# Kernel tuning notes

Hardware: AMD Instinct MI355X
Metric: run time of the kernel (lower is better)

The kernel has to match this reference:

```python
import jax, jax.numpy as jnp
import numpy as np

N = 1024      # num_nodes
D = 64        # input/hidden/output feature dim
IDX = 64      # idx_dim
H = 8         # msg MLP width
L = 3         # num_layers


def setup_inputs() -> dict:
    key = jax.random.key(0)
    ks = jax.random.split(key, 10)
    return {
        "y": jax.random.normal(ks[0], (N, D), jnp.float32),
        "adj": jax.random.uniform(ks[1], (N, N), jnp.float32),
        "adj_deriv": jax.random.normal(ks[2], (N, N), jnp.float32),
        "t_grad": jax.random.normal(ks[3], (N, N), jnp.float32),
        "idx_emb": jax.random.normal(ks[4], (N, IDX), jnp.float32),
        # stacked params for the two msg MLPs (index 0 = adj, 1 = adj_derivative)
        "msg_W1": jax.random.normal(ks[5], (2, H, 2 * IDX + 1), jnp.float32) / np.float32(np.sqrt(2 * IDX + 1)),
        "msg_b1": jnp.zeros((2, H), jnp.float32),
        "msg_W2": jax.random.normal(ks[6], (2, H, H), jnp.float32) / np.float32(np.sqrt(H)),
        "msg_b2": jnp.zeros((2, H), jnp.float32),
        "msg_W3": jax.random.normal(ks[7], (2, 1, H), jnp.float32) / np.float32(np.sqrt(H)),
        "msg_b3": jnp.zeros((2, 1), jnp.float32),
        # per-layer fusion weights: [A@x, A.T@x, dA@x, dA.T@x, x] -> 5 matrices
        "gnn_W": jax.random.normal(ks[8], (L, 5, D, D), jnp.float32) / np.float32(np.sqrt(D)),
        "gnn_b": jnp.zeros((L, D), jnp.float32),
    }


def _msg_mlp(a, idx_emb, W1, b1, W2, b2, W3, b3):
    # Edge-wise 2-hidden-layer relu MLP over concat([a_ij, emb_i, emb_j]).
    # Split W1 so the [N,N,2*IDX+1] concat is never materialized.
    w_a = W1[:, 0]                 # [H]
    w_i = W1[:, 1:1 + IDX]         # [H, IDX]
    w_j = W1[:, 1 + IDX:]          # [H, IDX]
    row = idx_emb @ w_i.T          # [N, H]
    col = idx_emb @ w_j.T          # [N, H]
    h = jax.nn.relu(a[:, :, None] * w_a + row[:, None, :] + col[None, :, :] + b1)  # [N,N,H]
    h = jax.nn.relu(jnp.einsum('nmh,kh->nmk', h, W2) + b2)                          # [N,N,H]
    out = jnp.einsum('nmh,oh->nmo', h, W3) + b3                                     # [N,N,1]
    return out[..., 0]


def reference(y, adj, adj_deriv, t_grad, idx_emb, msg_W1, msg_b1, msg_W2, msg_b2,
              msg_W3, msg_b3, gnn_W, gnn_b):
    # enc_idx=True: reweight adjacency and its derivative with the edge-wise MLPs
    a = _msg_mlp(adj, idx_emb, msg_W1[0], msg_b1[0], msg_W2[0], msg_b2[0], msg_W3[0], msg_b3[0])
    ad = _msg_mlp(adj_deriv, idx_emb, msg_W1[1], msg_b1[1], msg_W2[1], msg_b2[1], msg_W3[1], msg_b3[1])

    x = y
    for l in range(L):
        W, b = gnn_W[l], gnn_b[l]
        x = ((a @ x) @ W[0] + (a.T @ x) @ W[1]
             + (ad @ x) @ W[2] + (ad.T @ x) @ W[3]
             + x @ W[4] + b)
        if l < L - 1:
            x = jax.nn.relu(x)

    tg = jnp.mean(t_grad, axis=0)          # [N]
    return tg[:, None] * x                 # einsum('i,ij->ij')
```

## Files before the change

kernel.cpp:

```cpp
#include <hip/hip_runtime.h>

typedef __attribute__((ext_vector_type(8))) short bf16x8;
typedef __attribute__((ext_vector_type(4))) float f32x4;
typedef __attribute__((ext_vector_type(4))) unsigned short us4;

__device__ __forceinline__ unsigned short f2bf(float f) {
    unsigned int u = __builtin_bit_cast(unsigned int, f);
    unsigned int r = (u + 0x7fffu + ((u >> 16) & 1u)) >> 16;
    return (unsigned short)r;
}

__global__ __launch_bounds__(256) void k_aux(
    const float* __restrict__ idx_emb, const float* __restrict__ msg_W1,
    float* __restrict__ rc,
    const float* __restrict__ t_grad, float* __restrict__ tg,
    const float* __restrict__ y, unsigned short* __restrict__ xbf,
    const float* __restrict__ gnn_W, unsigned short* __restrict__ WbfT) {
    __shared__ float red[4][64];
    int bx = blockIdx.x, t = threadIdx.x;
    if (bx < 128) {
        int tid = bx * 256 + t;
        int h = tid & 7, n = (tid >> 3) & 1023, t_ = (tid >> 13) & 1, k = tid >> 14;
        const float* wv = msg_W1 + k * 1032 + h * 129 + 1 + t_ * 64;
        const float* e = idx_emb + n * 64;
        float s = 0.f;
#pragma unroll
        for (int d = 0; d < 64; ++d) s += e[d] * wv[d];
        rc[(k * 2 + t_) * 8192 + n * 8 + h] = s;
    } else if (bx < 144) {
        int jl = t & 63, sg = t >> 6;
        int j = (bx - 128) * 64 + jl;
        float acc = 0.f;
        for (int i = 0; i < 256; ++i) acc += t_grad[(sg * 256 + i) * 1024 + j];
        red[sg][jl] = acc;
        __syncthreads();
        if (sg == 0)
            tg[j] = (red[0][jl] + red[1][jl] + red[2][jl] + red[3][jl]) * (1.f / 1024.f);
    } else if (bx < 160) {
        int base = (bx - 144) * 4096 + t;
#pragma unroll
        for (int p = 0; p < 16; ++p) xbf[base + p * 256] = f2bf(y[base + p * 256]);
    } else if (bx < 175) {
        int wi = bx - 160;
        const float* src = gnn_W + wi * 4096;
        unsigned short* dst = WbfT + wi * 4096;
        int c = t & 63, dg = t >> 6;
#pragma unroll
        for (int p = 0; p < 16; ++p) {
            int d = dg + p * 4;
            dst[c * 64 + d] = f2bf(src[d * 64 + c]);
        }
    }
}

__global__ __launch_bounds__(256) void k_msgcvt(
    const float* __restrict__ adj, const float* __restrict__ adj_deriv,
    const float* __restrict__ W1, const float* __restrict__ b1,
    const float* __restrict__ W2, const float* __restrict__ b2,
    const float* __restrict__ W3, const float* __restrict__ b3,
    const float* __restrict__ rc, unsigned short* __restrict__ Abf) {
    int mt = blockIdx.x, nt = blockIdx.y, z = blockIdx.z;
    const float* A = z ? adj_deriv : adj;
    unsigned short* D0 = Abf + z * 2097152;
    unsigned short* D1 = D0 + 1048576;
    int k = z;

    float wa[8], b1v[8], w2[64], b2v[8], w3v[8];
#pragma unroll
    for (int h = 0; h < 8; ++h) {
        wa[h]  = W1[k * 1032 + h * 129];
        b1v[h] = b1[k * 8 + h];
        b2v[h] = b2[k * 8 + h];
        w3v[h] = W3[k * 8 + h];
    }
#pragma unroll
    for (int i = 0; i < 64; ++i) w2[i] = W2[k * 64 + i];
    float b3v = b3[k];

    int t = threadIdx.x;
    int c = t & 63, rg = t >> 6;
    const float* colp = rc + (k * 2 + 1) * 8192 + (mt * 64 + c) * 8;
    float cm[8];
    *(float4*)&cm[0] = *(const float4*)colp;
    *(float4*)&cm[4] = *(const float4*)(colp + 4);
    const float* rowp = rc + (k * 2) * 8192 + (nt * 64) * 8;

    __shared__ unsigned short tile[64][65];
#pragma unroll
    for (int p = 0; p < 16; ++p) {
        int r = rg + 4 * p;
        float av = A[(nt * 64 + r) * 1024 + mt * 64 + c];
        float rn[8];
        *(float4*)&rn[0] = *(const float4*)(rowp + r * 8);
        *(float4*)&rn[4] = *(const float4*)(rowp + r * 8 + 4);
        float h1[8];
#pragma unroll
        for (int h = 0; h < 8; ++h) {
            float v = av * wa[h] + rn[h] + cm[h] + b1v[h];
            h1[h] = v > 0.f ? v : 0.f;
        }
        float o = b3v;
#pragma unroll
        for (int kk = 0; kk < 8; ++kk) {
            float s = b2v[kk];
#pragma unroll
            for (int h = 0; h < 8; ++h) s += h1[h] * w2[kk * 8 + h];
            s = s > 0.f ? s : 0.f;
            o += s * w3v[kk];
        }
        unsigned short us = f2bf(o);
        D0[(nt * 64 + r) * 1024 + mt * 64 + c] = us;
        tile[r][c] = us;
    }
    __syncthreads();
#pragma unroll
    for (int p = 0; p < 16; ++p) {
        int r = rg + 4 * p;
        D1[(mt * 64 + r) * 1024 + nt * 64 + c] = tile[c][r];
    }
}

template<int L>
__global__ __launch_bounds__(256) void k_layer(
    const unsigned short* __restrict__ Abf,
    const unsigned short* __restrict__ xbf,
    const float* __restrict__ Pin, const float* __restrict__ u4in,
    const float* __restrict__ bprev,
    const unsigned short* __restrict__ WT,
    float* __restrict__ u4out, float* __restrict__ Pout) {
    int nt = blockIdx.x, ms = blockIdx.y;
    int t = threadIdx.x, w = t >> 6, l64 = t & 63;
    int lr = l64 & 15, lk = l64 >> 4, klo = 8 * lk;
    int m0 = ms * 64;
    __shared__ unsigned short uTs[16384];
    __shared__ unsigned short xs[4096];

    if constexpr (L == 0) {
#pragma unroll
        for (int p = 0; p < 2; ++p) {
            int e = (t + p * 256) * 8;
            *(bf16x8*)&xs[e] = *(const bf16x8*)&xbf[m0 * 64 + e];
        }
    } else {
#pragma unroll
        for (int p = 0; p < 4; ++p) {
            int q = t + p * 256;
            int row = q >> 4, c4 = (q & 15) * 4;
            int gi = (m0 + row) * 64 + c4;
            float4 acc4 = *(const float4*)&u4in[gi];
            float4 b4 = *(const float4*)&bprev[c4];
            acc4.x += b4.x; acc4.y += b4.y; acc4.z += b4.z; acc4.w += b4.w;
#pragma unroll
            for (int s = 0; s < 16; ++s) {
                float4 pv = *(const float4*)&Pin[s * 65536 + gi];
                acc4.x += pv.x; acc4.y += pv.y; acc4.z += pv.z; acc4.w += pv.w;
            }
            us4 pk;
            pk[0] = f2bf(fmaxf(acc4.x, 0.f));
            pk[1] = f2bf(fmaxf(acc4.y, 0.f));
            pk[2] = f2bf(fmaxf(acc4.z, 0.f));
            pk[3] = f2bf(fmaxf(acc4.w, 0.f));
            *(us4*)&xs[row * 64 + c4] = pk;
        }
    }
    __syncthreads();

    int mloc = w * 16 + lr;
    bf16x8 xa0 = *(const bf16x8*)&xs[mloc * 64 + klo];
    bf16x8 xa1 = *(const bf16x8*)&xs[mloc * 64 + 32 + klo];
    int njmax = (nt == 0) ? 5 : 4;
    for (int j = 0; j < njmax; ++j) {
        f32x4 au[4];
#pragma unroll
        for (int cf = 0; cf < 4; ++cf) au[cf] = (f32x4){0.f, 0.f, 0.f, 0.f};
#pragma unroll
        for (int cf = 0; cf < 4; ++cf) {
            bf16x8 wf0 = *(const bf16x8*)&WT[(j * 64 + cf * 16 + lr) * 64 + klo];
            bf16x8 wf1 = *(const bf16x8*)&WT[(j * 64 + cf * 16 + lr) * 64 + 32 + klo];
            au[cf] = __builtin_amdgcn_mfma_f32_16x16x32_bf16(xa0, wf0, au[cf], 0, 0, 0);
            au[cf] = __builtin_amdgcn_mfma_f32_16x16x32_bf16(xa1, wf1, au[cf], 0, 0, 0);
        }
        if (j < 4) {
#pragma unroll
            for (int cf = 0; cf < 4; ++cf) {
                int cc = cf * 16 + lr;
                us4 pk;
                pk[0] = f2bf(au[cf][0]); pk[1] = f2bf(au[cf][1]);
                pk[2] = f2bf(au[cf][2]); pk[3] = f2bf(au[cf][3]);
                int off = ((j * 64 + cc) * 64 + w * 16 + lk * 4) * 2;
                *(us4*)((char*)uTs + (off ^ ((cc & 7) << 4))) = pk;
            }
        } else {
#pragma unroll
            for (int cf = 0; cf < 4; ++cf)
#pragma unroll
                for (int r = 0; r < 4; ++r)
                    u4out[(m0 + w * 16 + lk * 4 + r) * 64 + cf * 16 + lr] = au[cf][r];
        }
    }
    __syncthreads();

    f32x4 acc[4];
#pragma unroll
    for (int cf = 0; cf < 4; ++cf) acc[cf] = (f32x4){0.f, 0.f, 0.f, 0.f};
    int arow = nt * 64 + w * 16 + lr;
#pragma unroll
    for (int j = 0; j < 4; ++j) {
#pragma unroll
        for (int kk = 0; kk < 2; ++kk) {
            bf16x8 af = *(const bf16x8*)&Abf[j * 1048576 + arow * 1024 + m0 + kk * 32 + klo];
#pragma unroll
            for (int cf = 0; cf < 4; ++cf) {
                int cc = cf * 16 + lr;
                int off = ((j * 64 + cc) * 64 + kk * 32 + klo) * 2;
                bf16x8 bfr = *(const bf16x8*)((char*)uTs + (off ^ ((cc & 7) << 4)));
                acc[cf] = __builtin_amdgcn_mfma_f32_16x16x32_bf16(af, bfr, acc[cf], 0, 0, 0);
            }
        }
    }
    float* Pp = Pout + ms * 65536;
    int nbase = nt * 64 + w * 16 + lk * 4;
#pragma unroll
    for (int cf = 0; cf < 4; ++cf)
#pragma unroll
        for (int r = 0; r < 4; ++r)
            Pp[(nbase + r) * 64 + cf * 16 + lr] = acc[cf][r];
}

__global__ void k_final(const float* __restrict__ P, const float* __restrict__ u4,
                        const float* __restrict__ b, const float* __restrict__ tg,
                        float* __restrict__ out) {
    int idx = blockIdx.x * 256 + threadIdx.x;
    int n = idx >> 6, c = idx & 63;
    float s = u4[idx] + b[c];
#pragma unroll
    for (int k = 0; k < 16; ++k) s += P[k * 65536 + idx];
    out[idx] = tg[n] * s;
}

extern "C" void kernel_launch(void* const* d_in, const int* in_sizes, int n_in,
                              void* d_out, int out_size, void* d_ws, size_t ws_size,
                              hipStream_t stream) {
    const float* y         = (const float*)d_in[0];
    const float* adj       = (const float*)d_in[1];
    const float* adj_deriv = (const float*)d_in[2];
    const float* t_grad    = (const float*)d_in[3];
    const float* idx_emb   = (const float*)d_in[4];
    const float* msg_W1    = (const float*)d_in[5];
    const float* msg_b1    = (const float*)d_in[6];
    const float* msg_W2    = (const float*)d_in[7];
    const float* msg_b2    = (const float*)d_in[8];
    const float* msg_W3    = (const float*)d_in[9];
    const float* msg_b3    = (const float*)d_in[10];
    const float* gnn_W     = (const float*)d_in[11];
    const float* gnn_b     = (const float*)d_in[12];
    float* outp = (float*)d_out;

    float* ws = (float*)d_ws;
    float* rc   = ws;
    float* tg   = ws + 32768;
    float* u4A  = ws + 33792;
    float* u4B  = ws + 99328;
    float* PA   = ws + 164864;
    float* PB   = ws + 1213440;
    unsigned short* xbf  = (unsigned short*)(ws + 2262016);
    unsigned short* WbfT = (unsigned short*)(ws + 2294784);
    unsigned short* Abf  = (unsigned short*)(ws + 2325504);

    k_aux<<<175, 256, 0, stream>>>(idx_emb, msg_W1, rc, t_grad, tg,
                                   y, xbf, gnn_W, WbfT);
    k_msgcvt<<<dim3(16, 16, 2), 256, 0, stream>>>(adj, adj_deriv,
                                                  msg_W1, msg_b1, msg_W2, msg_b2,
                                                  msg_W3, msg_b3, rc, Abf);
    k_layer<0><<<dim3(16, 16), 256, 0, stream>>>(Abf, xbf, PA, u4A, gnn_b,
                                                 WbfT, u4A, PA);
    k_layer<1><<<dim3(16, 16), 256, 0, stream>>>(Abf, xbf, PA, u4A, gnn_b,
                                                 WbfT + 20480, u4B, PB);
    k_layer<2><<<dim3(16, 16), 256, 0, stream>>>(Abf, xbf, PB, u4B, gnn_b + 64,
                                                 WbfT + 40960, u4A, PA);
    k_final<<<256, 256, 0, stream>>>(PA, u4A, gnn_b + 128, tg, outp);
}
```

Baseline: 73.10 us.

## Widen layer K-split to 256 columns per block, fold self term into partials

Each layer block now covers 256 source nodes in four chunks instead of 64, so the grid shrinks from 16x16 to 16x4 and the partial-sum buffers shrink from 16 slices to 4. The separate u4 (x@W4) output is gone. The diagonal block computes the self term straight into its accumulator, which reduces reduction traffic in the next layer and in the final kernel. In exchange there are only 64 blocks on a GPU with many CUs, so occupancy and parallelism drop, and each block does more serial work with extra barriers.

```diff
diff --git a/kernel.cpp b/kernel.cpp
--- a/kernel.cpp
+++ b/kernel.cpp
@@ -121,37 +121,35 @@
 }
 
 template<int L>
-__global__ __launch_bounds__(256) void k_layer(
+__global__ __launch_bounds__(256) void k_g(
     const unsigned short* __restrict__ Abf,
     const unsigned short* __restrict__ xbf,
-    const float* __restrict__ Pin, const float* __restrict__ u4in,
+    const unsigned short* __restrict__ WT,
     const float* __restrict__ bprev,
-    const unsigned short* __restrict__ WT,
-    float* __restrict__ u4out, float* __restrict__ Pout) {
+    const float* __restrict__ Pin,
+    float* __restrict__ Pout) {
     int nt = blockIdx.x, ms = blockIdx.y;
     int t = threadIdx.x, w = t >> 6, l64 = t & 63;
     int lr = l64 & 15, lk = l64 >> 4, klo = 8 * lk;
-    int m0 = ms * 64;
+    __shared__ unsigned short xs[16384];
     __shared__ unsigned short uTs[16384];
-    __shared__ unsigned short xs[4096];
 
     if constexpr (L == 0) {
 #pragma unroll
-        for (int p = 0; p < 2; ++p) {
-            int e = (t + p * 256) * 8;
-            *(bf16x8*)&xs[e] = *(const bf16x8*)&xbf[m0 * 64 + e];
+        for (int p = 0; p < 8; ++p) {
+            int q = t + p * 256;
+            int e = q * 8;
+            *(bf16x8*)&xs[e] = *(const bf16x8*)&xbf[ms * 16384 + e];
         }
     } else {
 #pragma unroll
-        for (int p = 0; p < 4; ++p) {
+        for (int p = 0; p < 16; ++p) {
             int q = t + p * 256;
             int row = q >> 4, c4 = (q & 15) * 4;
-            int gi = (m0 + row) * 64 + c4;
-            float4 acc4 = *(const float4*)&u4in[gi];
-            float4 b4 = *(const float4*)&bprev[c4];
-            acc4.x += b4.x; acc4.y += b4.y; acc4.z += b4.z; acc4.w += b4.w;
-#pragma unroll
-            for (int s = 0; s < 16; ++s) {
+            int gi = (ms * 256 + row) * 64 + c4;
+            float4 acc4 = *(const float4*)&bprev[c4];
+#pragma unroll
+            for (int s = 0; s < 4; ++s) {
                 float4 pv = *(const float4*)&Pin[s * 65536 + gi];
                 acc4.x += pv.x; acc4.y += pv.y; acc4.z += pv.z; acc4.w += pv.w;
             }
@@ -165,22 +163,42 @@
     }
     __syncthreads();
 
-    int mloc = w * 16 + lr;
-    bf16x8 xa0 = *(const bf16x8*)&xs[mloc * 64 + klo];
-    bf16x8 xa1 = *(const bf16x8*)&xs[mloc * 64 + 32 + klo];
-    int njmax = (nt == 0) ? 5 : 4;
-    for (int j = 0; j < njmax; ++j) {
-        f32x4 au[4];
-#pragma unroll
-        for (int cf = 0; cf < 4; ++cf) au[cf] = (f32x4){0.f, 0.f, 0.f, 0.f};
-#pragma unroll
-        for (int cf = 0; cf < 4; ++cf) {
-            bf16x8 wf0 = *(const bf16x8*)&WT[(j * 64 + cf * 16 + lr) * 64 + klo];
-            bf16x8 wf1 = *(const bf16x8*)&WT[(j * 64 + cf * 16 + lr) * 64 + 32 + klo];
-            au[cf] = __builtin_amdgcn_mfma_f32_16x16x32_bf16(xa0, wf0, au[cf], 0, 0, 0);
-            au[cf] = __builtin_amdgcn_mfma_f32_16x16x32_bf16(xa1, wf1, au[cf], 0, 0, 0);
-        }
-        if (j < 4) {
+    f32x4 acc[4];
+#pragma unroll
+    for (int cf = 0; cf < 4; ++cf) acc[cf] = (f32x4){0.f, 0.f, 0.f, 0.f};
+
+    if (ms == (nt >> 2)) {
+        const unsigned short* W4 = WT + 16384;
+        int xrow = (nt & 3) * 64 + w * 16 + lr;
+#pragma unroll
+        for (int kk = 0; kk < 2; ++kk) {
+            bf16x8 af = *(const bf16x8*)&xs[xrow * 64 + kk * 32 + klo];
+#pragma unroll
+            for (int cf = 0; cf < 4; ++cf) {
+                bf16x8 bfr = *(const bf16x8*)&W4[(cf * 16 + lr) * 64 + kk * 32 + klo];
+                acc[cf] = __builtin_amdgcn_mfma_f32_16x16x32_bf16(af, bfr, acc[cf], 0, 0, 0);
+            }
+        }
+    }
+
+    int arow = nt * 64 + w * 16 + lr;
+    for (int ch = 0; ch < 4; ++ch) {
+        if (ch > 0) __syncthreads();
+        int mloc = ch * 64 + w * 16 + lr;
+        bf16x8 xa0 = *(const bf16x8*)&xs[mloc * 64 + klo];
+        bf16x8 xa1 = *(const bf16x8*)&xs[mloc * 64 + 32 + klo];
+#pragma unroll
+        for (int j = 0; j < 4; ++j) {
+            f32x4 au[4];
+#pragma unroll
+            for (int cf = 0; cf < 4; ++cf) au[cf] = (f32x4){0.f, 0.f, 0.f, 0.f};
+#pragma unroll
+            for (int cf = 0; cf < 4; ++cf) {
+                bf16x8 wf0 = *(const bf16x8*)&WT[(j * 64 + cf * 16 + lr) * 64 + klo];
+                bf16x8 wf1 = *(const bf16x8*)&WT[(j * 64 + cf * 16 + lr) * 64 + 32 + klo];
+                au[cf] = __builtin_amdgcn_mfma_f32_16x16x32_bf16(xa0, wf0, au[cf], 0, 0, 0);
+                au[cf] = __builtin_amdgcn_mfma_f32_16x16x32_bf16(xa1, wf1, au[cf], 0, 0, 0);
+            }
 #pragma unroll
             for (int cf = 0; cf < 4; ++cf) {
                 int cc = cf * 16 + lr;
@@ -190,34 +208,26 @@
                 int off = ((j * 64 + cc) * 64 + w * 16 + lk * 4) * 2;
                 *(us4*)((char*)uTs + (off ^ ((cc & 7) << 4))) = pk;
             }
-        } else {
-#pragma unroll
-            for (int cf = 0; cf < 4; ++cf)
-#pragma unroll
-                for (int r = 0; r < 4; ++r)
-                    u4out[(m0 + w * 16 + lk * 4 + r) * 64 + cf * 16 + lr] = au[cf][r];
-        }
-    }
-    __syncthreads();
-
-    f32x4 acc[4];
-#pragma unroll
-    for (int cf = 0; cf < 4; ++cf) acc[cf] = (f32x4){0.f, 0.f, 0.f, 0.f};
-    int arow = nt * 64 + w * 16 + lr;
-#pragma unroll
-    for (int j = 0; j < 4; ++j) {
-#pragma unroll
-        for (int kk = 0; kk < 2; ++kk) {
-            bf16x8 af = *(const bf16x8*)&Abf[j * 1048576 + arow * 1024 + m0 + kk * 32 + klo];
-#pragma unroll
-            for (int cf = 0; cf < 4; ++cf) {
-                int cc = cf * 16 + lr;
-                int off = ((j * 64 + cc) * 64 + kk * 32 + klo) * 2;
-                bf16x8 bfr = *(const bf16x8*)((char*)uTs + (off ^ ((cc & 7) << 4)));
-                acc[cf] = __builtin_amdgcn_mfma_f32_16x16x32_bf16(af, bfr, acc[cf], 0, 0, 0);
-            }
-        }
-    }
+        }
+        __syncthreads();
+
+        int m0 = ms * 256 + ch * 64;
+#pragma unroll
+        for (int j = 0; j < 4; ++j) {
+#pragma unroll
+            for (int kk = 0; kk < 2; ++kk) {
+                bf16x8 af = *(const bf16x8*)&Abf[j * 1048576 + arow * 1024 + m0 + kk * 32 + klo];
+#pragma unroll
+                for (int cf = 0; cf < 4; ++cf) {
+                    int cc = cf * 16 + lr;
+                    int off = ((j * 64 + cc) * 64 + kk * 32 + klo) * 2;
+                    bf16x8 bfr = *(const bf16x8*)((char*)uTs + (off ^ ((cc & 7) << 4)));
+                    acc[cf] = __builtin_amdgcn_mfma_f32_16x16x32_bf16(af, bfr, acc[cf], 0, 0, 0);
+                }
+            }
+        }
+    }
+
     float* Pp = Pout + ms * 65536;
     int nbase = nt * 64 + w * 16 + lk * 4;
 #pragma unroll
@@ -227,14 +237,13 @@
             Pp[(nbase + r) * 64 + cf * 16 + lr] = acc[cf][r];
 }
 
-__global__ void k_final(const float* __restrict__ P, const float* __restrict__ u4,
-                        const float* __restrict__ b, const float* __restrict__ tg,
-                        float* __restrict__ out) {
+__global__ void k_postf(const float* __restrict__ P, const float* __restrict__ b,
+                        const float* __restrict__ tg, float* __restrict__ out) {
     int idx = blockIdx.x * 256 + threadIdx.x;
     int n = idx >> 6, c = idx & 63;
-    float s = u4[idx] + b[c];
-#pragma unroll
-    for (int k = 0; k < 16; ++k) s += P[k * 65536 + idx];
+    float s = b[c];
+#pragma unroll
+    for (int k = 0; k < 4; ++k) s += P[k * 65536 + idx];
     out[idx] = tg[n] * s;
 }
 
@@ -257,26 +266,24 @@
     float* outp = (float*)d_out;
 
     float* ws = (float*)d_ws;
-    float* rc   = ws;
-    float* tg   = ws + 32768;
-    float* u4A  = ws + 33792;
-    float* u4B  = ws + 99328;
-    float* PA   = ws + 164864;
-    float* PB   = ws + 1213440;
-    unsigned short* xbf  = (unsigned short*)(ws + 2262016);
-    unsigned short* WbfT = (unsigned short*)(ws + 2294784);
-    unsigned short* Abf  = (unsigned short*)(ws + 2325504);
+    float* rc = ws;
+    float* tg = ws + 32768;
+    float* PA = ws + 33792;
+    float* PB = ws + 295936;
+    unsigned short* xbfA = (unsigned short*)(ws + 558080);
+    unsigned short* WbfT = (unsigned short*)(ws + 590848);
+    unsigned short* Abf  = (unsigned short*)(ws + 621568);
 
     k_aux<<<175, 256, 0, stream>>>(idx_emb, msg_W1, rc, t_grad, tg,
-                                   y, xbf, gnn_W, WbfT);
+                                   y, xbfA, gnn_W, WbfT);
     k_msgcvt<<<dim3(16, 16, 2), 256, 0, stream>>>(adj, adj_deriv,
                                                   msg_W1, msg_b1, msg_W2, msg_b2,
                                                   msg_W3, msg_b3, rc, Abf);
-    k_layer<0><<<dim3(16, 16), 256, 0, stream>>>(Abf, xbf, PA, u4A, gnn_b,
-                                                 WbfT, u4A, PA);
-    k_layer<1><<<dim3(16, 16), 256, 0, stream>>>(Abf, xbf, PA, u4A, gnn_b,
-                                                 WbfT + 20480, u4B, PB);
-    k_layer<2><<<dim3(16, 16), 256, 0, stream>>>(Abf, xbf, PB, u4B, gnn_b + 64,
-                                                 WbfT + 40960, u4A, PA);
-    k_final<<<256, 256, 0, stream>>>(PA, u4A, gnn_b + 128, tg, outp);
-}
+    k_g<0><<<dim3(16, 4), 256, 0, stream>>>(Abf, xbfA, WbfT,
+                                            gnn_b, PA, PA);
+    k_g<1><<<dim3(16, 4), 256, 0, stream>>>(Abf, xbfA, WbfT + 20480,
+                                            gnn_b, PA, PB);
+    k_g<2><<<dim3(16, 4), 256, 0, stream>>>(Abf, xbfA, WbfT + 40960,
+                                            gnn_b + 64, PB, PA);
+    k_postf<<<256, 256, 0, stream>>>(PA, gnn_b + 128, tg, outp);
+}
```

After: 95.51 us. 30.7% more time.
